# Kernel optimization log

Measured on AMD Instinct MI355X. Metric: run time of the kernel, lower is better.

Reference implementation:

```python
import jax, jax.numpy as jnp
import numpy as np

IN_F = 256
OUT_F = 256
ALPHA = 0.2  # leaky-relu slope
NEG_INF = -9e15


def setup_inputs() -> dict:
    key = jax.random.key(0)
    ks = jax.random.split(key, 8)
    N_e, N_kc = 10000, 2000
    exercise_h = jax.random.normal(ks[0], (N_e, IN_F), dtype=jnp.float32)
    kc_h = jax.random.normal(ks[1], (N_kc, IN_F), dtype=jnp.float32)
    adj = jax.random.randint(ks[2], (N_e, N_kc), 0, 2, dtype=jnp.int32)
    # parameters (kaiming-ish scaling)
    W1 = jax.random.normal(ks[3], (IN_F, OUT_F), dtype=jnp.float32) * np.sqrt(2.0 / IN_F)
    E = jax.random.normal(ks[4], (IN_F, OUT_F), dtype=jnp.float32) * np.sqrt(2.0 / IN_F)
    a = jax.random.normal(ks[5], (2 * OUT_F, 1), dtype=jnp.float32) * np.sqrt(2.0 / (2 * OUT_F))
    rd_w = jax.random.normal(ks[6], (OUT_F, 2 * OUT_F), dtype=jnp.float32) * np.sqrt(2.0 / (2 * OUT_F))
    rd_b = jnp.zeros((OUT_F,), dtype=jnp.float32)
    return {"exercise_h": exercise_h, "kc_h": kc_h, "adj": adj,
            "W1": W1, "E": E, "a": a, "rd_w": rd_w, "rd_b": rd_b}


def reference(exercise_h, kc_h, adj, W1, E, a, rd_w, rd_b):
    kc_Wh = kc_h @ W1            # [N_kc, D]
    ex_Wh = exercise_h @ W1      # [N_e, D]
    # a . concat(ex_Wh_i, kc_Wh_j) == a1.ex_Wh_i + a2.kc_Wh_j  (avoids [N_e,N_kc,2D] tensor)
    a1 = a[:OUT_F, 0]
    a2 = a[OUT_F:, 0]
    e = jax.nn.leaky_relu((ex_Wh @ a1)[:, None] + (kc_Wh @ a2)[None, :], negative_slope=ALPHA)  # [N_e, N_kc]
    logits = jnp.where(adj > 0, e, jnp.float32(NEG_INF))
    attention = jax.nn.softmax(logits, axis=1)
    new_kc = attention @ kc_Wh           # [N_e, D]
    ex_Eh = exercise_h @ E               # [N_e, D]
    feat = jnp.concatenate([new_kc, new_kc * ex_Eh], axis=1)  # [N_e, 2D]
    out = feat @ rd_w.T + rd_b
    return jax.nn.elu(out)
```

## Files before the change

### kernel.cpp

```cpp
#include <hip/hip_runtime.h>

#define N_E 10000
#define N_KC 2000
#define ALPHA 0.2f

typedef __attribute__((ext_vector_type(8))) short short8;
typedef __attribute__((ext_vector_type(4))) float f32x4;

__device__ float g_w1a1[256];
__device__ float g_t[2048];
__device__ __align__(16) unsigned short g_W1T_pk[16 * 8 * 512];
__device__ __align__(16) unsigned short g_ET_pk[16 * 8 * 512];
__device__ __align__(16) unsigned short g_rdw_pk[16 * 16 * 512];
__device__ __align__(16) unsigned short g_kcWh_pk[16 * 64 * 512];

__device__ __forceinline__ unsigned short f2bf(float f) {
  union { float f; unsigned int u; } v; v.f = f;
  unsigned int r = v.u + 0x7FFFu + ((v.u >> 16) & 1u);
  return (unsigned short)(r >> 16);
}

__device__ __forceinline__ void cvt_store4(float4 v, unsigned short* dst) {
  ushort4 o;
  o.x = f2bf(v.x); o.y = f2bf(v.y); o.z = f2bf(v.z); o.w = f2bf(v.w);
  *reinterpret_cast<ushort4*>(dst) = o;
}

__global__ __launch_bounds__(256) void prep_kernel(
    const float* __restrict__ W1, const float* __restrict__ E,
    const float* __restrict__ a, const float* __restrict__ rd_w) {
  int b = blockIdx.x, tid = threadIdx.x;
  if (b < 32) {
#pragma unroll
    for (int s2 = 0; s2 < 2; ++s2) {
      int sId = b * 512 + tid + s2 * 256;
      int ct = sId >> 10, rem = sId & 1023;
      int kt = rem >> 6, lane = rem & 63;
      int g = lane >> 4, r = lane & 15;
      const float* src = rd_w + (size_t)(ct * 16 + r) * 512 + kt * 32 + g * 8;
      unsigned short* dst = g_rdw_pk + (size_t)sId * 8;
      cvt_store4(*(const float4*)src, dst);
      cvt_store4(*(const float4*)(src + 4), dst + 4);
    }
  } else if (b < 48) {
#pragma unroll
    for (int s2 = 0; s2 < 2; ++s2) {
      int sId = (b - 32) * 512 + tid + s2 * 256;
      int ct = sId >> 9, rem = sId & 511;
      int kt = rem >> 6, lane = rem & 63;
      int g = lane >> 4, r = lane & 15;
      int col = ct * 16 + r, k = kt * 32 + g * 8;
      unsigned short* dst = g_W1T_pk + (size_t)sId * 8;
      ushort4 o0, o1;
      o0.x = f2bf(W1[(k + 0) * 256 + col]); o0.y = f2bf(W1[(k + 1) * 256 + col]);
      o0.z = f2bf(W1[(k + 2) * 256 + col]); o0.w = f2bf(W1[(k + 3) * 256 + col]);
      o1.x = f2bf(W1[(k + 4) * 256 + col]); o1.y = f2bf(W1[(k + 5) * 256 + col]);
      o1.z = f2bf(W1[(k + 6) * 256 + col]); o1.w = f2bf(W1[(k + 7) * 256 + col]);
      *(ushort4*)dst = o0; *(ushort4*)(dst + 4) = o1;
    }
  } else if (b < 64) {
#pragma unroll
    for (int s2 = 0; s2 < 2; ++s2) {
      int sId = (b - 48) * 512 + tid + s2 * 256;
      int ct = sId >> 9, rem = sId & 511;
      int kt = rem >> 6, lane = rem & 63;
      int g = lane >> 4, r = lane & 15;
      int col = ct * 16 + r, k = kt * 32 + g * 8;
      unsigned short* dst = g_ET_pk + (size_t)sId * 8;
      ushort4 o0, o1;
      o0.x = f2bf(E[(k + 0) * 256 + col]); o0.y = f2bf(E[(k + 1) * 256 + col]);
      o0.z = f2bf(E[(k + 2) * 256 + col]); o0.w = f2bf(E[(k + 3) * 256 + col]);
      o1.x = f2bf(E[(k + 4) * 256 + col]); o1.y = f2bf(E[(k + 5) * 256 + col]);
      o1.z = f2bf(E[(k + 6) * 256 + col]); o1.w = f2bf(E[(k + 7) * 256 + col]);
      *(ushort4*)dst = o0; *(ushort4*)(dst + 4) = o1;
    }
  } else if (b == 64) {
    float acc = 0.f;
    for (int q = 0; q < 64; ++q) {
      float4 wv = *(const float4*)(W1 + (size_t)tid * 256 + q * 4);
      float4 a4 = *(const float4*)(a + q * 4);
      acc += wv.x * a4.x + wv.y * a4.y + wv.z * a4.z + wv.w * a4.w;
    }
    g_w1a1[tid] = acc;
  } else {
    for (int idx = tid; idx < 16 * 2 * 512; idx += 256) {
      int ct = idx >> 10, rem = idx & 1023;
      int kt = 62 + (rem >> 9), off = rem & 511;
      g_kcWh_pk[((size_t)ct * 64 + kt) * 512 + off] = 0;
    }
    if (tid < 48) g_t[2000 + tid] = 0.f;
  }
}

__global__ __launch_bounds__(256) void kc_mfma_kernel(
    const float* __restrict__ kc_h, const float* __restrict__ a) {
  __shared__ float tred[4][4][4];
  int tid = threadIdx.x, lane = tid & 63, w = tid >> 6;
  int r = lane & 15, g = lane >> 4;
  int j0 = blockIdx.x * 16;
  f32x4 acc[4] = {{0.f,0.f,0.f,0.f},{0.f,0.f,0.f,0.f},
                  {0.f,0.f,0.f,0.f},{0.f,0.f,0.f,0.f}};
  for (int kk = 0; kk < 8; ++kk) {
    int k = kk * 32 + g * 8;
    const float* src = kc_h + (size_t)(j0 + r) * 256 + k;
    float4 x0 = *(const float4*)src, x1 = *(const float4*)(src + 4);
    short8 af = {(short)f2bf(x0.x), (short)f2bf(x0.y), (short)f2bf(x0.z),
                 (short)f2bf(x0.w), (short)f2bf(x1.x), (short)f2bf(x1.y),
                 (short)f2bf(x1.z), (short)f2bf(x1.w)};
#pragma unroll
    for (int n = 0; n < 4; ++n) {
      short8 bf = *(const short8*)(g_W1T_pk + ((size_t)(w * 4 + n) * 8 + kk) *
                                                  512 + lane * 8);
      acc[n] = __builtin_amdgcn_mfma_f32_16x16x32_bf16(af, bf, acc[n], 0, 0, 0);
    }
  }
  int j = j0 + g * 4;
  int kt = j >> 5, lsub = ((j >> 3) & 3) * 16 + r, sub = (g & 1) * 4;
#pragma unroll
  for (int n = 0; n < 4; ++n) {
    int ct = w * 4 + n;
    ushort4 o;
    o.x = f2bf(acc[n][0]); o.y = f2bf(acc[n][1]);
    o.z = f2bf(acc[n][2]); o.w = f2bf(acc[n][3]);
    *reinterpret_cast<ushort4*>(
        g_kcWh_pk + ((size_t)ct * 64 + kt) * 512 + lsub * 8 + sub) = o;
  }
  float a2v[4];
#pragma unroll
  for (int n = 0; n < 4; ++n) a2v[n] = a[256 + w * 64 + n * 16 + r];
  float tp[4];
#pragma unroll
  for (int q = 0; q < 4; ++q)
    tp[q] = acc[0][q] * a2v[0] + acc[1][q] * a2v[1] + acc[2][q] * a2v[2] +
            acc[3][q] * a2v[3];
#pragma unroll
  for (int off = 1; off < 16; off <<= 1)
#pragma unroll
    for (int q = 0; q < 4; ++q) tp[q] += __shfl_xor(tp[q], off, 64);
  if (r == 0)
#pragma unroll
    for (int q = 0; q < 4; ++q) tred[w][g][q] = tp[q];
  __syncthreads();
  if (tid < 16)
    g_t[j0 + tid] = tred[0][tid >> 2][tid & 3] + tred[1][tid >> 2][tid & 3] +
                    tred[2][tid >> 2][tid & 3] + tred[3][tid >> 2][tid & 3];
}

#define PSTR 264
#define FST 536
__global__ __launch_bounds__(512, 8) void main_kernel(
    const float* __restrict__ exh, const int* __restrict__ adj,
    const float* __restrict__ rd_b, float* __restrict__ out) {
  __shared__ __align__(16) unsigned char smem[33280];
  __shared__ float ds_part[8][16];
  __shared__ float red16[16];
  float* t_s = (float*)smem;
  unsigned short* p_s = (unsigned short*)(smem + 8192);
  unsigned short* exh_pk_s = (unsigned short*)(smem + 25088);
  unsigned short* feat_s = (unsigned short*)smem;

  int tid = threadIdx.x, w = tid >> 6, lane = tid & 63;
  int r = lane & 15, g = lane >> 4;
  int i0 = blockIdx.x * 16;

  const int* arow = adj + (size_t)(i0 + r) * N_KC;

  int4 pa0 = *(const int4*)(arow + w * 32 + g * 8);
  int4 pa1 = *(const int4*)(arow + w * 32 + g * 8 + 4);

  ((float4*)t_s)[tid] = ((const float4*)g_t)[tid];
  {
    const float* wsrc = g_w1a1 + w * 32 + g * 8;
    float4 w0 = *(const float4*)wsrc, w1 = *(const float4*)(wsrc + 4);
    const float* xsrc = exh + (size_t)(i0 + r) * 256 + w * 32 + g * 8;
    float4 x0 = *(const float4*)xsrc, x1 = *(const float4*)(xsrc + 4);
    unsigned short* dst = exh_pk_s + w * 512 + lane * 8;
    cvt_store4(x0, dst); cvt_store4(x1, dst + 4);
    float sp = x0.x * w0.x + x0.y * w0.y + x0.z * w0.z + x0.w * w0.w +
               x1.x * w1.x + x1.y * w1.y + x1.z * w1.z + x1.w * w1.w;
    sp += __shfl_xor(sp, 16, 64);
    sp += __shfl_xor(sp, 32, 64);
    if (lane < 16) ds_part[w][lane] = sp;
  }
  __syncthreads();
  if (tid < 16) {
    float s = 0.f;
#pragma unroll
    for (int ww = 0; ww < 8; ++ww) s += ds_part[ww][tid];
    red16[tid] = s;
  }
  __syncthreads();
  float sv = red16[r];

  f32x4 accP[2] = {{0.f,0.f,0.f,0.f},{0.f,0.f,0.f,0.f}};
  float dsum = 0.f;

  auto gen = [&](int c, int4 a0v, int4 a1v) {
    int kk = c * 8 + w;
    int c0 = kk * 32 + g * 8;
    int4 pk = {0, 0, 0, 0};
    if (kk < 63 && c0 < N_KC) {
      float4 t0 = *(const float4*)(t_s + c0);
      float4 t1 = *(const float4*)(t_s + c0 + 4);
      float tv[8] = {t0.x, t0.y, t0.z, t0.w, t1.x, t1.y, t1.z, t1.w};
      int av[8] = {a0v.x, a0v.y, a0v.z, a0v.w, a1v.x, a1v.y, a1v.z, a1v.w};
      unsigned ub[8];
#pragma unroll
      for (int j = 0; j < 8; ++j) {
        float x = sv + tv[j];
        float lx = fmaxf(x, ALPHA * x);
        float pv = (av[j] > 0) ? __expf(lx) : 0.f;
        dsum += pv;
        ub[j] = __float_as_uint(pv) + 0x8000u;
      }
      pk.x = (int)((ub[0] >> 16) | (ub[1] & 0xFFFF0000u));
      pk.y = (int)((ub[2] >> 16) | (ub[3] & 0xFFFF0000u));
      pk.z = (int)((ub[4] >> 16) | (ub[5] & 0xFFFF0000u));
      pk.w = (int)((ub[6] >> 16) | (ub[7] & 0xFFFF0000u));
    }
    *(int4*)(p_s + ((size_t)((c & 1) * 16 + r)) * PSTR + w * 32 + g * 8) = pk;
  };

  auto mfma_chunk = [&](int c) {
    const unsigned short* pb = p_s + (size_t)(c & 1) * 16 * PSTR;
    const unsigned short* bb =
        g_kcWh_pk + ((size_t)(w * 2) * 64 + c * 8) * 512 + lane * 8;
#pragma unroll
    for (int u = 0; u < 8; ++u) {
      short8 av = *(const short8*)(pb + (size_t)r * PSTR + u * 32 + g * 8);
      short8 b0 = *(const short8*)(bb + u * 512);
      short8 b1 = *(const short8*)(bb + 64 * 512 + u * 512);
      accP[0] = __builtin_amdgcn_mfma_f32_16x16x32_bf16(av, b0, accP[0], 0, 0, 0);
      accP[1] = __builtin_amdgcn_mfma_f32_16x16x32_bf16(av, b1, accP[1], 0, 0, 0);
    }
  };

  int4 na0 = {0, 0, 0, 0}, na1 = {0, 0, 0, 0};
  for (int c = 0; c < 8; ++c) {
    if (c < 7) {
      int kk = (c + 1) * 8 + w, c0 = kk * 32 + g * 8;
      if (kk < 63 && c0 < N_KC) {
        na0 = *(const int4*)(arow + c0);
        na1 = *(const int4*)(arow + c0 + 4);
      }
    }
    gen(c, pa0, pa1);
    if (c > 0) mfma_chunk(c - 1);
    __syncthreads();
    pa0 = na0; pa1 = na1;
  }
  mfma_chunk(7);

  dsum += __shfl_xor(dsum, 16, 64);
  dsum += __shfl_xor(dsum, 32, 64);
  if (lane < 16) ds_part[w][lane] = dsum;

  f32x4 accE[2] = {{0.f,0.f,0.f,0.f},{0.f,0.f,0.f,0.f}};
#pragma unroll
  for (int kk = 0; kk < 8; ++kk) {
    short8 a0 = *(const short8*)(exh_pk_s + kk * 512 + lane * 8);
#pragma unroll
    for (int n = 0; n < 2; ++n) {
      short8 bf = *(const short8*)(g_ET_pk + ((size_t)(w * 2 + n) * 8 + kk) *
                                                 512 + lane * 8);
      accE[n] = __builtin_amdgcn_mfma_f32_16x16x32_bf16(a0, bf, accE[n], 0, 0, 0);
    }
  }
  __syncthreads();
  if (tid < 16) {
    float s = 0.f;
#pragma unroll
    for (int ww = 0; ww < 8; ++ww) s += ds_part[ww][tid];
    red16[tid] = 1.f / fmaxf(s, 1e-30f);
  }
  __syncthreads();

#pragma unroll
  for (int n = 0; n < 2; ++n) {
    int col = w * 32 + n * 16 + r;
#pragma unroll
    for (int q = 0; q < 4; ++q) {
      int row = g * 4 + q;
      float nk = accP[n][q] * red16[row];
      feat_s[(size_t)row * FST + col] = f2bf(nk);
      feat_s[(size_t)row * FST + 256 + col] = f2bf(nk * accE[n][q]);
    }
  }
  __syncthreads();

  f32x4 accO[2] = {{0.f,0.f,0.f,0.f},{0.f,0.f,0.f,0.f}};
#pragma unroll
  for (int kt = 0; kt < 16; ++kt) {
    int k = kt * 32 + g * 8;
    short8 a0 = *(const short8*)(feat_s + (size_t)r * FST + k);
#pragma unroll
    for (int n = 0; n < 2; ++n) {
      short8 bf = *(const short8*)(g_rdw_pk + ((size_t)(w * 2 + n) * 16 + kt) *
                                                  512 + lane * 8);
      accO[n] = __builtin_amdgcn_mfma_f32_16x16x32_bf16(a0, bf, accO[n], 0, 0, 0);
    }
  }
#pragma unroll
  for (int n = 0; n < 2; ++n) {
    int col = w * 32 + n * 16 + r;
    float bias = rd_b[col];
#pragma unroll
    for (int q = 0; q < 4; ++q) {
      int row = i0 + g * 4 + q;
      float x = accO[n][q] + bias;
      float res = x > 0.f ? x : (__expf(x) - 1.f);
      out[(size_t)row * 256 + col] = res;
    }
  }
}

extern "C" void kernel_launch(void* const* d_in, const int* in_sizes, int n_in,
                              void* d_out, int out_size, void* d_ws,
                              size_t ws_size, hipStream_t stream) {
  const float* exh  = (const float*)d_in[0];
  const float* kc_h = (const float*)d_in[1];
  const int*   adj  = (const int*)d_in[2];
  const float* W1   = (const float*)d_in[3];
  const float* E    = (const float*)d_in[4];
  const float* a    = (const float*)d_in[5];
  const float* rd_w = (const float*)d_in[6];
  const float* rd_b = (const float*)d_in[7];
  float* out = (float*)d_out;

  prep_kernel<<<66, 256, 0, stream>>>(W1, E, a, rd_w);
  kc_mfma_kernel<<<N_KC / 16, 256, 0, stream>>>(kc_h, a);
  main_kernel<<<(N_E + 15) / 16, 512, 0, stream>>>(exh, adj, rd_b, out);
}
```

Measured before the change: 190.6 us.

## Process 32 rows per block and feed attention weights straight into MFMA registers

Each block now handles 32 exercise rows, with two row halves each split across four column-group waves. Every wave generates its own attention-probability fragment directly in registers and feeds it to the MFMA, which removes the shared-memory staging buffer and the per-chunk barriers. The softmax denominator is reduced inside one wave instead of across the block. The trade-off is that each wave now recomputes the exp for its rows (four times redundantly), the adj reads sit serially in a loop of 63 steps, and the launch-bounds occupancy hint is halved.

```diff
diff --git a/kernel.cpp b/kernel.cpp
--- a/kernel.cpp
+++ b/kernel.cpp
@@ -146,170 +146,164 @@
                     tred[2][tid >> 2][tid & 3] + tred[3][tid >> 2][tid & 3];
 }
 
-#define PSTR 264
 #define FST 536
-__global__ __launch_bounds__(512, 8) void main_kernel(
+__global__ __launch_bounds__(512, 4) void main_kernel(
     const float* __restrict__ exh, const int* __restrict__ adj,
     const float* __restrict__ rd_b, float* __restrict__ out) {
-  __shared__ __align__(16) unsigned char smem[33280];
-  __shared__ float ds_part[8][16];
-  __shared__ float red16[16];
+  __shared__ __align__(16) unsigned char smem[34816];
+  __shared__ float ds_part[8][32];
+  __shared__ float red32[32];
+  __shared__ float inv32[32];
   float* t_s = (float*)smem;
-  unsigned short* p_s = (unsigned short*)(smem + 8192);
-  unsigned short* exh_pk_s = (unsigned short*)(smem + 25088);
+  unsigned short* exh_pk_s = (unsigned short*)(smem + 8192);
   unsigned short* feat_s = (unsigned short*)smem;
 
   int tid = threadIdx.x, w = tid >> 6, lane = tid & 63;
   int r = lane & 15, g = lane >> 4;
-  int i0 = blockIdx.x * 16;
-
-  const int* arow = adj + (size_t)(i0 + r) * N_KC;
-
-  int4 pa0 = *(const int4*)(arow + w * 32 + g * 8);
-  int4 pa1 = *(const int4*)(arow + w * 32 + g * 8 + 4);
+  int i0 = blockIdx.x * 32;
+  int mh = w >> 2;
+  int cg = w & 3;
 
   ((float4*)t_s)[tid] = ((const float4*)g_t)[tid];
   {
     const float* wsrc = g_w1a1 + w * 32 + g * 8;
     float4 w0 = *(const float4*)wsrc, w1 = *(const float4*)(wsrc + 4);
-    const float* xsrc = exh + (size_t)(i0 + r) * 256 + w * 32 + g * 8;
-    float4 x0 = *(const float4*)xsrc, x1 = *(const float4*)(xsrc + 4);
-    unsigned short* dst = exh_pk_s + w * 512 + lane * 8;
-    cvt_store4(x0, dst); cvt_store4(x1, dst + 4);
-    float sp = x0.x * w0.x + x0.y * w0.y + x0.z * w0.z + x0.w * w0.w +
-               x1.x * w1.x + x1.y * w1.y + x1.z * w1.z + x1.w * w1.w;
-    sp += __shfl_xor(sp, 16, 64);
-    sp += __shfl_xor(sp, 32, 64);
-    if (lane < 16) ds_part[w][lane] = sp;
-  }
-  __syncthreads();
-  if (tid < 16) {
+    float sp[2];
+#pragma unroll
+    for (int m = 0; m < 2; ++m) {
+      int row = i0 + m * 16 + r; row = row < N_E ? row : N_E - 1;
+      const float* xsrc = exh + (size_t)row * 256 + w * 32 + g * 8;
+      float4 x0 = *(const float4*)xsrc, x1 = *(const float4*)(xsrc + 4);
+      unsigned short* dst = exh_pk_s + m * 4096 + w * 512 + lane * 8;
+      cvt_store4(x0, dst); cvt_store4(x1, dst + 4);
+      sp[m] = x0.x * w0.x + x0.y * w0.y + x0.z * w0.z + x0.w * w0.w +
+              x1.x * w1.x + x1.y * w1.y + x1.z * w1.z + x1.w * w1.w;
+      sp[m] += __shfl_xor(sp[m], 16, 64);
+      sp[m] += __shfl_xor(sp[m], 32, 64);
+    }
+    if (lane < 16) { ds_part[w][lane] = sp[0]; ds_part[w][16 + lane] = sp[1]; }
+  }
+  __syncthreads();
+  if (tid < 32) {
     float s = 0.f;
 #pragma unroll
     for (int ww = 0; ww < 8; ++ww) s += ds_part[ww][tid];
-    red16[tid] = s;
-  }
-  __syncthreads();
-  float sv = red16[r];
-
-  f32x4 accP[2] = {{0.f,0.f,0.f,0.f},{0.f,0.f,0.f,0.f}};
+    red32[tid] = s;
+  }
+  __syncthreads();
+  float sv = red32[mh * 16 + r];
+
+  int grow = i0 + mh * 16 + r; grow = grow < N_E ? grow : N_E - 1;
+  const int* arow = adj + (size_t)grow * N_KC;
+
+  f32x4 accP[4] = {{0.f,0.f,0.f,0.f},{0.f,0.f,0.f,0.f},
+                   {0.f,0.f,0.f,0.f},{0.f,0.f,0.f,0.f}};
   float dsum = 0.f;
 
-  auto gen = [&](int c, int4 a0v, int4 a1v) {
-    int kk = c * 8 + w;
-    int c0 = kk * 32 + g * 8;
-    int4 pk = {0, 0, 0, 0};
-    if (kk < 63 && c0 < N_KC) {
-      float4 t0 = *(const float4*)(t_s + c0);
-      float4 t1 = *(const float4*)(t_s + c0 + 4);
-      float tv[8] = {t0.x, t0.y, t0.z, t0.w, t1.x, t1.y, t1.z, t1.w};
-      int av[8] = {a0v.x, a0v.y, a0v.z, a0v.w, a1v.x, a1v.y, a1v.z, a1v.w};
-      unsigned ub[8];
-#pragma unroll
-      for (int j = 0; j < 8; ++j) {
-        float x = sv + tv[j];
-        float lx = fmaxf(x, ALPHA * x);
-        float pv = (av[j] > 0) ? __expf(lx) : 0.f;
-        dsum += pv;
-        ub[j] = __float_as_uint(pv) + 0x8000u;
+  int4 pa0 = *(const int4*)(arow + g * 8);
+  int4 pa1 = *(const int4*)(arow + g * 8 + 4);
+  float4 tc0 = *(const float4*)(t_s + g * 8);
+  float4 tc1 = *(const float4*)(t_s + g * 8 + 4);
+  const unsigned short* bbase = g_kcWh_pk + (size_t)lane * 8;
+
+#pragma unroll 1
+  for (int kk = 0; kk < 63; ++kk) {
+    short8 b0 = *(const short8*)(bbase + ((size_t)((cg * 4 + 0) * 64 + kk)) * 512);
+    short8 b1 = *(const short8*)(bbase + ((size_t)((cg * 4 + 1) * 64 + kk)) * 512);
+    short8 b2 = *(const short8*)(bbase + ((size_t)((cg * 4 + 2) * 64 + kk)) * 512);
+    short8 b3 = *(const short8*)(bbase + ((size_t)((cg * 4 + 3) * 64 + kk)) * 512);
+    int4 na0 = {0, 0, 0, 0}, na1 = {0, 0, 0, 0};
+    float4 tn0 = {0.f,0.f,0.f,0.f}, tn1 = {0.f,0.f,0.f,0.f};
+    if (kk < 62) {
+      int nc0 = (kk + 1) * 32 + g * 8;
+      if (nc0 + 8 <= N_KC) {
+        na0 = *(const int4*)(arow + nc0);
+        na1 = *(const int4*)(arow + nc0 + 4);
       }
-      pk.x = (int)((ub[0] >> 16) | (ub[1] & 0xFFFF0000u));
-      pk.y = (int)((ub[2] >> 16) | (ub[3] & 0xFFFF0000u));
-      pk.z = (int)((ub[4] >> 16) | (ub[5] & 0xFFFF0000u));
-      pk.w = (int)((ub[6] >> 16) | (ub[7] & 0xFFFF0000u));
-    }
-    *(int4*)(p_s + ((size_t)((c & 1) * 16 + r)) * PSTR + w * 32 + g * 8) = pk;
-  };
-
-  auto mfma_chunk = [&](int c) {
-    const unsigned short* pb = p_s + (size_t)(c & 1) * 16 * PSTR;
-    const unsigned short* bb =
-        g_kcWh_pk + ((size_t)(w * 2) * 64 + c * 8) * 512 + lane * 8;
-#pragma unroll
-    for (int u = 0; u < 8; ++u) {
-      short8 av = *(const short8*)(pb + (size_t)r * PSTR + u * 32 + g * 8);
-      short8 b0 = *(const short8*)(bb + u * 512);
-      short8 b1 = *(const short8*)(bb + 64 * 512 + u * 512);
-      accP[0] = __builtin_amdgcn_mfma_f32_16x16x32_bf16(av, b0, accP[0], 0, 0, 0);
-      accP[1] = __builtin_amdgcn_mfma_f32_16x16x32_bf16(av, b1, accP[1], 0, 0, 0);
-    }
-  };
-
-  int4 na0 = {0, 0, 0, 0}, na1 = {0, 0, 0, 0};
-  for (int c = 0; c < 8; ++c) {
-    if (c < 7) {
-      int kk = (c + 1) * 8 + w, c0 = kk * 32 + g * 8;
-      if (kk < 63 && c0 < N_KC) {
-        na0 = *(const int4*)(arow + c0);
-        na1 = *(const int4*)(arow + c0 + 4);
-      }
-    }
-    gen(c, pa0, pa1);
-    if (c > 0) mfma_chunk(c - 1);
-    __syncthreads();
-    pa0 = na0; pa1 = na1;
-  }
-  mfma_chunk(7);
+      tn0 = *(const float4*)(t_s + nc0);
+      tn1 = *(const float4*)(t_s + nc0 + 4);
+    }
+    float tv[8] = {tc0.x, tc0.y, tc0.z, tc0.w, tc1.x, tc1.y, tc1.z, tc1.w};
+    int av[8] = {pa0.x, pa0.y, pa0.z, pa0.w, pa1.x, pa1.y, pa1.z, pa1.w};
+    unsigned ub[8];
+#pragma unroll
+    for (int j = 0; j < 8; ++j) {
+      float x = sv + tv[j];
+      float lx = fmaxf(x, ALPHA * x);
+      float pv = __expf(lx);
+      pv = (av[j] > 0) ? pv : 0.f;
+      dsum += pv;
+      ub[j] = __float_as_uint(pv) + 0x8000u;
+    }
+    union { unsigned u[4]; short8 s8; } pk;
+    pk.u[0] = (ub[0] >> 16) | (ub[1] & 0xFFFF0000u);
+    pk.u[1] = (ub[2] >> 16) | (ub[3] & 0xFFFF0000u);
+    pk.u[2] = (ub[4] >> 16) | (ub[5] & 0xFFFF0000u);
+    pk.u[3] = (ub[6] >> 16) | (ub[7] & 0xFFFF0000u);
+    short8 af = pk.s8;
+    accP[0] = __builtin_amdgcn_mfma_f32_16x16x32_bf16(af, b0, accP[0], 0, 0, 0);
+    accP[1] = __builtin_amdgcn_mfma_f32_16x16x32_bf16(af, b1, accP[1], 0, 0, 0);
+    accP[2] = __builtin_amdgcn_mfma_f32_16x16x32_bf16(af, b2, accP[2], 0, 0, 0);
+    accP[3] = __builtin_amdgcn_mfma_f32_16x16x32_bf16(af, b3, accP[3], 0, 0, 0);
+    pa0 = na0; pa1 = na1; tc0 = tn0; tc1 = tn1;
+  }
 
   dsum += __shfl_xor(dsum, 16, 64);
   dsum += __shfl_xor(dsum, 32, 64);
-  if (lane < 16) ds_part[w][lane] = dsum;
-
-  f32x4 accE[2] = {{0.f,0.f,0.f,0.f},{0.f,0.f,0.f,0.f}};
+  if (cg == 0 && lane < 16) inv32[mh * 16 + lane] = 1.f / fmaxf(dsum, 1e-30f);
+
+  f32x4 accE[4] = {{0.f,0.f,0.f,0.f},{0.f,0.f,0.f,0.f},
+                   {0.f,0.f,0.f,0.f},{0.f,0.f,0.f,0.f}};
 #pragma unroll
   for (int kk = 0; kk < 8; ++kk) {
-    short8 a0 = *(const short8*)(exh_pk_s + kk * 512 + lane * 8);
-#pragma unroll
-    for (int n = 0; n < 2; ++n) {
-      short8 bf = *(const short8*)(g_ET_pk + ((size_t)(w * 2 + n) * 8 + kk) *
+    short8 a0 = *(const short8*)(exh_pk_s + mh * 4096 + kk * 512 + lane * 8);
+#pragma unroll
+    for (int n = 0; n < 4; ++n) {
+      short8 bf = *(const short8*)(g_ET_pk + ((size_t)((cg * 4 + n) * 8 + kk)) *
                                                  512 + lane * 8);
       accE[n] = __builtin_amdgcn_mfma_f32_16x16x32_bf16(a0, bf, accE[n], 0, 0, 0);
     }
   }
   __syncthreads();
-  if (tid < 16) {
-    float s = 0.f;
-#pragma unroll
-    for (int ww = 0; ww < 8; ++ww) s += ds_part[ww][tid];
-    red16[tid] = 1.f / fmaxf(s, 1e-30f);
-  }
-  __syncthreads();
-
-#pragma unroll
-  for (int n = 0; n < 2; ++n) {
-    int col = w * 32 + n * 16 + r;
+
+#pragma unroll
+  for (int n = 0; n < 4; ++n) {
+    int col = cg * 64 + n * 16 + r;
 #pragma unroll
     for (int q = 0; q < 4; ++q) {
-      int row = g * 4 + q;
-      float nk = accP[n][q] * red16[row];
+      int row = mh * 16 + g * 4 + q;
+      float nk = accP[n][q] * inv32[row];
       feat_s[(size_t)row * FST + col] = f2bf(nk);
       feat_s[(size_t)row * FST + 256 + col] = f2bf(nk * accE[n][q]);
     }
   }
   __syncthreads();
 
-  f32x4 accO[2] = {{0.f,0.f,0.f,0.f},{0.f,0.f,0.f,0.f}};
+  f32x4 accO[4] = {{0.f,0.f,0.f,0.f},{0.f,0.f,0.f,0.f},
+                   {0.f,0.f,0.f,0.f},{0.f,0.f,0.f,0.f}};
 #pragma unroll
   for (int kt = 0; kt < 16; ++kt) {
     int k = kt * 32 + g * 8;
-    short8 a0 = *(const short8*)(feat_s + (size_t)r * FST + k);
-#pragma unroll
-    for (int n = 0; n < 2; ++n) {
-      short8 bf = *(const short8*)(g_rdw_pk + ((size_t)(w * 2 + n) * 16 + kt) *
+    short8 a0 = *(const short8*)(feat_s + (size_t)(mh * 16 + r) * FST + k);
+#pragma unroll
+    for (int n = 0; n < 4; ++n) {
+      short8 bf = *(const short8*)(g_rdw_pk + ((size_t)((cg * 4 + n) * 16 + kt)) *
                                                   512 + lane * 8);
       accO[n] = __builtin_amdgcn_mfma_f32_16x16x32_bf16(a0, bf, accO[n], 0, 0, 0);
     }
   }
-#pragma unroll
-  for (int n = 0; n < 2; ++n) {
-    int col = w * 32 + n * 16 + r;
-    float bias = rd_b[col];
-#pragma unroll
-    for (int q = 0; q < 4; ++q) {
-      int row = i0 + g * 4 + q;
-      float x = accO[n][q] + bias;
-      float res = x > 0.f ? x : (__expf(x) - 1.f);
-      out[(size_t)row * 256 + col] = res;
+  if (i0 + mh * 16 < N_E) {
+#pragma unroll
+    for (int n = 0; n < 4; ++n) {
+      int col = cg * 64 + n * 16 + r;
+      float bias = rd_b[col];
+#pragma unroll
+      for (int q = 0; q < 4; ++q) {
+        int row = i0 + mh * 16 + g * 4 + q;
+        float x = accO[n][q] + bias;
+        float res = x > 0.f ? x : (__expf(x) - 1.f);
+        out[(size_t)row * 256 + col] = res;
+      }
     }
   }
 }
@@ -329,5 +323,5 @@
 
   prep_kernel<<<66, 256, 0, stream>>>(W1, E, a, rd_w);
   kc_mfma_kernel<<<N_KC / 16, 256, 0, stream>>>(kc_h, a);
-  main_kernel<<<(N_E + 15) / 16, 512, 0, stream>>>(exh, adj, rd_b, out);
-}
+  main_kernel<<<(N_E + 31) / 32, 512, 0, stream>>>(exh, adj, rd_b, out);
+}
```

New measurement: 261.0 us. 36.9% more time.

## Generate full attention tile into swizzled LDS, then run one MFMA pass

Applied to the files above, without the earlier changes.

The interleaved gen/MFMA loop with double-buffered P chunks and a barrier per chunk is replaced. Now all 63 K-slices of the bf16 attention tile are generated up front into a 63 KB XOR-swizzled LDS buffer. Each warp owns two rows, so the row sums reduce within a warp via shuffles instead of cross-warp shared reductions. A single barrier then precedes a 63-step MFMA loop that uses dual accumulators to break the dependency chains. The cost is much larger LDS (launch bounds drop from 8 to 2 blocks), lost overlap between adjacency loads and MFMA, and exh being reloaded from global for the E projection.

```diff
diff --git a/kernel.cpp b/kernel.cpp
--- a/kernel.cpp
+++ b/kernel.cpp
@@ -146,142 +146,132 @@
                     tred[2][tid >> 2][tid & 3] + tred[3][tid >> 2][tid & 3];
 }
 
-#define PSTR 264
 #define FST 536
-__global__ __launch_bounds__(512, 8) void main_kernel(
+__global__ __launch_bounds__(512, 2) void main_kernel(
     const float* __restrict__ exh, const int* __restrict__ adj,
     const float* __restrict__ rd_b, float* __restrict__ out) {
-  __shared__ __align__(16) unsigned char smem[33280];
-  __shared__ float ds_part[8][16];
-  __shared__ float red16[16];
-  float* t_s = (float*)smem;
-  unsigned short* p_s = (unsigned short*)(smem + 8192);
-  unsigned short* exh_pk_s = (unsigned short*)(smem + 25088);
+  __shared__ __align__(16) unsigned char smem[64512 + 8192];
+  __shared__ float sv_s[16];
+  __shared__ float inv_s[16];
+  unsigned short* P_lds = (unsigned short*)smem;
+  float* t_s = (float*)(smem + 64512);
   unsigned short* feat_s = (unsigned short*)smem;
 
   int tid = threadIdx.x, w = tid >> 6, lane = tid & 63;
-  int r = lane & 15, g = lane >> 4;
   int i0 = blockIdx.x * 16;
-
-  const int* arow = adj + (size_t)(i0 + r) * N_KC;
-
-  int4 pa0 = *(const int4*)(arow + w * 32 + g * 8);
-  int4 pa1 = *(const int4*)(arow + w * 32 + g * 8 + 4);
 
   ((float4*)t_s)[tid] = ((const float4*)g_t)[tid];
   {
-    const float* wsrc = g_w1a1 + w * 32 + g * 8;
+    int row = tid >> 5, seg = tid & 31;
+    const float* xsrc = exh + (size_t)(i0 + row) * 256 + seg * 8;
+    float4 x0 = *(const float4*)xsrc, x1 = *(const float4*)(xsrc + 4);
+    const float* wsrc = g_w1a1 + seg * 8;
     float4 w0 = *(const float4*)wsrc, w1 = *(const float4*)(wsrc + 4);
-    const float* xsrc = exh + (size_t)(i0 + r) * 256 + w * 32 + g * 8;
-    float4 x0 = *(const float4*)xsrc, x1 = *(const float4*)(xsrc + 4);
-    unsigned short* dst = exh_pk_s + w * 512 + lane * 8;
-    cvt_store4(x0, dst); cvt_store4(x1, dst + 4);
     float sp = x0.x * w0.x + x0.y * w0.y + x0.z * w0.z + x0.w * w0.w +
                x1.x * w1.x + x1.y * w1.y + x1.z * w1.z + x1.w * w1.w;
+    sp += __shfl_xor(sp, 1, 64);
+    sp += __shfl_xor(sp, 2, 64);
+    sp += __shfl_xor(sp, 4, 64);
+    sp += __shfl_xor(sp, 8, 64);
     sp += __shfl_xor(sp, 16, 64);
-    sp += __shfl_xor(sp, 32, 64);
-    if (lane < 16) ds_part[w][lane] = sp;
-  }
-  __syncthreads();
-  if (tid < 16) {
-    float s = 0.f;
-#pragma unroll
-    for (int ww = 0; ww < 8; ++ww) s += ds_part[ww][tid];
-    red16[tid] = s;
-  }
-  __syncthreads();
-  float sv = red16[r];
-
-  f32x4 accP[2] = {{0.f,0.f,0.f,0.f},{0.f,0.f,0.f,0.f}};
-  float dsum = 0.f;
-
-  auto gen = [&](int c, int4 a0v, int4 a1v) {
-    int kk = c * 8 + w;
-    int c0 = kk * 32 + g * 8;
-    int4 pk = {0, 0, 0, 0};
-    if (kk < 63 && c0 < N_KC) {
-      float4 t0 = *(const float4*)(t_s + c0);
-      float4 t1 = *(const float4*)(t_s + c0 + 4);
-      float tv[8] = {t0.x, t0.y, t0.z, t0.w, t1.x, t1.y, t1.z, t1.w};
-      int av[8] = {a0v.x, a0v.y, a0v.z, a0v.w, a1v.x, a1v.y, a1v.z, a1v.w};
-      unsigned ub[8];
-#pragma unroll
-      for (int j = 0; j < 8; ++j) {
-        float x = sv + tv[j];
-        float lx = fmaxf(x, ALPHA * x);
-        float pv = (av[j] > 0) ? __expf(lx) : 0.f;
-        dsum += pv;
-        ub[j] = __float_as_uint(pv) + 0x8000u;
+    if ((tid & 31) == 0) sv_s[row] = sp;
+  }
+  __syncthreads();
+
+  {
+    int kks = lane >> 2, g = lane & 3;
+    float dsum[2] = {0.f, 0.f};
+#pragma unroll
+    for (int rr = 0; rr < 2; ++rr) {
+      int row = w * 2 + rr;
+      float svr = sv_s[row];
+      const int* arow = adj + (size_t)(i0 + row) * N_KC;
+#pragma unroll
+      for (int v = 0; v < 4; ++v) {
+        int kk = v * 16 + kks;
+        int c0 = kk * 32 + g * 8;
+        int4 a0v = {0, 0, 0, 0}, a1v = {0, 0, 0, 0};
+        if (c0 + 4 <= N_KC) a0v = *(const int4*)(arow + c0);
+        if (c0 + 8 <= N_KC) a1v = *(const int4*)(arow + c0 + 4);
+        float4 t0 = *(const float4*)(t_s + c0);
+        float4 t1 = *(const float4*)(t_s + c0 + 4);
+        float tv[8] = {t0.x, t0.y, t0.z, t0.w, t1.x, t1.y, t1.z, t1.w};
+        int av[8] = {a0v.x, a0v.y, a0v.z, a0v.w, a1v.x, a1v.y, a1v.z, a1v.w};
+        unsigned ub[8];
+#pragma unroll
+        for (int j = 0; j < 8; ++j) {
+          float x = svr + tv[j];
+          float lx = fmaxf(x, ALPHA * x);
+          float pv = (av[j] > 0) ? __expf(lx) : 0.f;
+          dsum[rr] += pv;
+          ub[j] = __float_as_uint(pv) + 0x8000u;
+        }
+        int4 pk;
+        pk.x = (int)((ub[0] >> 16) | (ub[1] & 0xFFFF0000u));
+        pk.y = (int)((ub[2] >> 16) | (ub[3] & 0xFFFF0000u));
+        pk.z = (int)((ub[4] >> 16) | (ub[5] & 0xFFFF0000u));
+        pk.w = (int)((ub[6] >> 16) | (ub[7] & 0xFFFF0000u));
+        if (kk < 63) {
+          int slot = (row ^ kks) | (g << 4);
+          *(int4*)(P_lds + ((size_t)kk << 9) + (slot << 3)) = pk;
+        }
       }
-      pk.x = (int)((ub[0] >> 16) | (ub[1] & 0xFFFF0000u));
-      pk.y = (int)((ub[2] >> 16) | (ub[3] & 0xFFFF0000u));
-      pk.z = (int)((ub[4] >> 16) | (ub[5] & 0xFFFF0000u));
-      pk.w = (int)((ub[6] >> 16) | (ub[7] & 0xFFFF0000u));
-    }
-    *(int4*)(p_s + ((size_t)((c & 1) * 16 + r)) * PSTR + w * 32 + g * 8) = pk;
-  };
-
-  auto mfma_chunk = [&](int c) {
-    const unsigned short* pb = p_s + (size_t)(c & 1) * 16 * PSTR;
-    const unsigned short* bb =
-        g_kcWh_pk + ((size_t)(w * 2) * 64 + c * 8) * 512 + lane * 8;
-#pragma unroll
-    for (int u = 0; u < 8; ++u) {
-      short8 av = *(const short8*)(pb + (size_t)r * PSTR + u * 32 + g * 8);
-      short8 b0 = *(const short8*)(bb + u * 512);
-      short8 b1 = *(const short8*)(bb + 64 * 512 + u * 512);
-      accP[0] = __builtin_amdgcn_mfma_f32_16x16x32_bf16(av, b0, accP[0], 0, 0, 0);
-      accP[1] = __builtin_amdgcn_mfma_f32_16x16x32_bf16(av, b1, accP[1], 0, 0, 0);
-    }
-  };
-
-  int4 na0 = {0, 0, 0, 0}, na1 = {0, 0, 0, 0};
-  for (int c = 0; c < 8; ++c) {
-    if (c < 7) {
-      int kk = (c + 1) * 8 + w, c0 = kk * 32 + g * 8;
-      if (kk < 63 && c0 < N_KC) {
-        na0 = *(const int4*)(arow + c0);
-        na1 = *(const int4*)(arow + c0 + 4);
-      }
-    }
-    gen(c, pa0, pa1);
-    if (c > 0) mfma_chunk(c - 1);
-    __syncthreads();
-    pa0 = na0; pa1 = na1;
-  }
-  mfma_chunk(7);
-
-  dsum += __shfl_xor(dsum, 16, 64);
-  dsum += __shfl_xor(dsum, 32, 64);
-  if (lane < 16) ds_part[w][lane] = dsum;
-
+    }
+#pragma unroll
+    for (int rr = 0; rr < 2; ++rr) {
+      float d = dsum[rr];
+      d += __shfl_xor(d, 1, 64);
+      d += __shfl_xor(d, 2, 64);
+      d += __shfl_xor(d, 4, 64);
+      d += __shfl_xor(d, 8, 64);
+      d += __shfl_xor(d, 16, 64);
+      d += __shfl_xor(d, 32, 64);
+      if (lane == 0) inv_s[w * 2 + rr] = 1.f / fmaxf(d, 1e-30f);
+    }
+  }
+  __syncthreads();
+
+  f32x4 accP[2][2] = {{{0.f,0.f,0.f,0.f},{0.f,0.f,0.f,0.f}},
+                      {{0.f,0.f,0.f,0.f},{0.f,0.f,0.f,0.f}}};
+  const unsigned short* bb0 =
+      g_kcWh_pk + (size_t)(w * 2 + 0) * 64 * 512 + lane * 8;
+  const unsigned short* bb1 =
+      g_kcWh_pk + (size_t)(w * 2 + 1) * 64 * 512 + lane * 8;
+#pragma unroll 7
+  for (int kk = 0; kk < 63; ++kk) {
+    short8 a = *(const short8*)(P_lds + ((size_t)kk << 9) +
+                                ((lane ^ (kk & 15)) << 3));
+    short8 b0 = *(const short8*)(bb0 + ((size_t)kk << 9));
+    short8 b1 = *(const short8*)(bb1 + ((size_t)kk << 9));
+    accP[0][kk & 1] = __builtin_amdgcn_mfma_f32_16x16x32_bf16(a, b0, accP[0][kk & 1], 0, 0, 0);
+    accP[1][kk & 1] = __builtin_amdgcn_mfma_f32_16x16x32_bf16(a, b1, accP[1][kk & 1], 0, 0, 0);
+  }
+
+  int r2 = lane & 15, g2 = lane >> 4;
   f32x4 accE[2] = {{0.f,0.f,0.f,0.f},{0.f,0.f,0.f,0.f}};
 #pragma unroll
-  for (int kk = 0; kk < 8; ++kk) {
-    short8 a0 = *(const short8*)(exh_pk_s + kk * 512 + lane * 8);
+  for (int kk8 = 0; kk8 < 8; ++kk8) {
+    const float* xs = exh + (size_t)(i0 + r2) * 256 + kk8 * 32 + g2 * 8;
+    float4 x0 = *(const float4*)xs, x1 = *(const float4*)(xs + 4);
+    short8 a0 = {(short)f2bf(x0.x), (short)f2bf(x0.y), (short)f2bf(x0.z),
+                 (short)f2bf(x0.w), (short)f2bf(x1.x), (short)f2bf(x1.y),
+                 (short)f2bf(x1.z), (short)f2bf(x1.w)};
 #pragma unroll
     for (int n = 0; n < 2; ++n) {
-      short8 bf = *(const short8*)(g_ET_pk + ((size_t)(w * 2 + n) * 8 + kk) *
+      short8 bf = *(const short8*)(g_ET_pk + ((size_t)(w * 2 + n) * 8 + kk8) *
                                                  512 + lane * 8);
       accE[n] = __builtin_amdgcn_mfma_f32_16x16x32_bf16(a0, bf, accE[n], 0, 0, 0);
     }
   }
   __syncthreads();
-  if (tid < 16) {
-    float s = 0.f;
-#pragma unroll
-    for (int ww = 0; ww < 8; ++ww) s += ds_part[ww][tid];
-    red16[tid] = 1.f / fmaxf(s, 1e-30f);
-  }
-  __syncthreads();
 
 #pragma unroll
   for (int n = 0; n < 2; ++n) {
-    int col = w * 32 + n * 16 + r;
+    int col = w * 32 + n * 16 + r2;
 #pragma unroll
     for (int q = 0; q < 4; ++q) {
-      int row = g * 4 + q;
-      float nk = accP[n][q] * red16[row];
+      int row = g2 * 4 + q;
+      float nk = (accP[n][0][q] + accP[n][1][q]) * inv_s[row];
       feat_s[(size_t)row * FST + col] = f2bf(nk);
       feat_s[(size_t)row * FST + 256 + col] = f2bf(nk * accE[n][q]);
     }
@@ -291,8 +281,8 @@
   f32x4 accO[2] = {{0.f,0.f,0.f,0.f},{0.f,0.f,0.f,0.f}};
 #pragma unroll
   for (int kt = 0; kt < 16; ++kt) {
-    int k = kt * 32 + g * 8;
-    short8 a0 = *(const short8*)(feat_s + (size_t)r * FST + k);
+    int k = kt * 32 + g2 * 8;
+    short8 a0 = *(const short8*)(feat_s + (size_t)r2 * FST + k);
 #pragma unroll
     for (int n = 0; n < 2; ++n) {
       short8 bf = *(const short8*)(g_rdw_pk + ((size_t)(w * 2 + n) * 16 + kt) *
@@ -302,11 +292,11 @@
   }
 #pragma unroll
   for (int n = 0; n < 2; ++n) {
-    int col = w * 32 + n * 16 + r;
+    int col = w * 32 + n * 16 + r2;
     float bias = rd_b[col];
 #pragma unroll
     for (int q = 0; q < 4; ++q) {
-      int row = i0 + g * 4 + q;
+      int row = i0 + g2 * 4 + q;
       float x = accO[n][q] + bias;
       float res = x > 0.f ? x : (__expf(x) - 1.f);
       out[(size_t)row * 256 + col] = res;
@@ -329,5 +319,5 @@
 
   prep_kernel<<<66, 256, 0, stream>>>(W1, E, a, rd_w);
   kc_mfma_kernel<<<N_KC / 16, 256, 0, stream>>>(kc_h, a);
-  main_kernel<<<(N_E + 15) / 16, 512, 0, stream>>>(exh, adj, rd_b, out);
-}
+  main_kernel<<<N_E / 16, 512, 0, stream>>>(exh, adj, rd_b, out);
+}
```

New measurement: 218.4 us. +14.6%, slower.
